# Performance work log

Measured on AMD Instinct MI355X. Metric: run time of the kernel, lower is better.

Reference implementation:

```python
import jax, jax.numpy as jnp
import numpy as np

N_NODES = 50000
N_EDGES = 800000
IN_CH, HID_CH, OUT_CH = 128, 128, 64


def _gcn_conv(x, W, b, src, dst, n):
    """PyG GCNConv: self-loops + symmetric norm + linear + scatter-add + bias."""
    loop = jnp.arange(n, dtype=src.dtype)
    src_sl = jnp.concatenate([src, loop])  # [E+N]
    dst_sl = jnp.concatenate([dst, loop])
    # degree computed on edges incl. self-loops (edge weight 1)
    deg = jax.ops.segment_sum(jnp.ones_like(dst_sl, dtype=x.dtype), dst_sl,
                              num_segments=n)
    dinv = jnp.where(deg > 0, jax.lax.rsqrt(deg), 0.0)
    norm = dinv[src_sl] * dinv[dst_sl]  # [E+N]
    xw = x @ W  # [N, F_out]
    msg = xw[src_sl] * norm[:, None]  # gather + scale, [E+N, F_out]
    out = jax.ops.segment_sum(msg, dst_sl, num_segments=n)
    return out + b


def setup_inputs() -> dict:
    key = jax.random.key(0)
    ks = jax.random.split(key, 5)
    x = jax.random.normal(ks[0], (N_NODES, IN_CH), dtype=jnp.float32)
    edge_index = jax.random.randint(ks[1], (2, N_EDGES), 0, N_NODES, dtype=jnp.int64)
    s1 = 1.0 / np.sqrt(IN_CH)
    s2 = 1.0 / np.sqrt(HID_CH)
    W1 = jax.random.normal(ks[2], (IN_CH, HID_CH), dtype=jnp.float32) * s1
    W2 = jax.random.normal(ks[3], (HID_CH, HID_CH), dtype=jnp.float32) * s2
    W3 = jax.random.normal(ks[4], (HID_CH, OUT_CH), dtype=jnp.float32) * s2
    return {
        "x": x, "edge_index": edge_index,
        "W1": W1, "b1": jnp.zeros((HID_CH,), jnp.float32),
        "W2": W2, "b2": jnp.zeros((HID_CH,), jnp.float32),
        "W3": W3, "b3": jnp.zeros((OUT_CH,), jnp.float32),
    }


def reference(x, edge_index, W1, b1, W2, b2, W3, b3):
    n = x.shape[0]
    src, dst = edge_index[0], edge_index[1]
    # dropout(p=0.6) is identity in eval mode
    h = jax.nn.relu(_gcn_conv(x, W1, b1, src, dst, n))
    h = jax.nn.relu(_gcn_conv(h, W2, b2, src, dst, n))
    out = _gcn_conv(h, W3, b3, src, dst, n)
    return out
```

## Files before the change

### kernel.cpp

```cpp
#include <hip/hip_runtime.h>
#include <cstdint>

#define CAP 32768
#define CHUNK 2048

typedef __attribute__((ext_vector_type(8))) short bf8_t;
typedef __attribute__((ext_vector_type(4))) float f4_t;

__device__ __forceinline__ uint32_t f_to_bf(float f) {
    union { float f; uint32_t u; } v; v.f = f;
    uint32_t u = v.u;
    return (u + 0x7fffu + ((u >> 16) & 1u)) >> 16;
}
__device__ __forceinline__ float bf_to_f(uint32_t h) {
    union { uint32_t u; float f; } v; v.u = h << 16; return v.f;
}
__device__ __forceinline__ float2 bf2_to_f2(uint32_t u) {
    union { uint32_t u; float f; } a, b;
    a.u = u << 16; b.u = u & 0xffff0000u;
    float2 r; r.x = a.f; r.y = b.f; return r;
}

__device__ __forceinline__ int detect64(const int* __restrict__ e32) {
    return (e32[1] | e32[3] | e32[5] | e32[7]) == 0;
}
__device__ __forceinline__ int edge_at(const void* edges, int is64, int idx) {
    if (is64) return (int)((const long long*)edges)[idx];
    return ((const int*)edges)[idx];
}

__global__ __launch_bounds__(256) void prep_kernel(
    const float* __restrict__ W1, const float* __restrict__ W2,
    const float* __restrict__ W3,
    uint16_t* w1h, uint16_t* w1l, uint16_t* w2h, uint16_t* w2l,
    uint16_t* w3h, uint16_t* w3l, int* __restrict__ bucket_cur) {
    if (blockIdx.x == 160) {
        if (threadIdx.x < 64) bucket_cur[threadIdx.x] = threadIdx.x * CAP;
        return;
    }
    int idx = blockIdx.x * 256 + threadIdx.x;
    const float* W; uint16_t* oh; uint16_t* ol; int FOUT; int e;
    if (idx < 16384)      { W = W1; oh = w1h; ol = w1l; FOUT = 128; e = idx; }
    else if (idx < 32768) { W = W2; oh = w2h; ol = w2l; FOUT = 128; e = idx - 16384; }
    else                  { W = W3; oh = w3h; ol = w3l; FOUT = 64;  e = idx - 32768; }
    int j = e & 7;
    int lane = (e >> 3) & 63;
    int rem = e >> 9;
    int NT = FOUT >> 4;
    int nt = rem % NT, kc = rem / NT;
    int k = kc * 32 + ((lane >> 4) << 3) + j;
    int c = nt * 16 + (lane & 15);
    float v = W[(size_t)k * FOUT + c];
    uint32_t h = f_to_bf(v);
    uint32_t l = f_to_bf(v - bf_to_f(h));
    oh[e] = (uint16_t)h;
    ol[e] = (uint16_t)l;
}

__device__ __forceinline__ void gemm1_body(
    const float* __restrict__ A, const uint16_t* __restrict__ Wfhi,
    const uint16_t* __restrict__ Wflo, uint16_t* __restrict__ Yout,
    int n, int cp, int tile0, int tstride, int lane) {
    constexpr int NT = 8, NTW = 2;
    int ntiles = (n + 15) >> 4;
    bf8_t wh[NTW][4], wl[NTW][4];
#pragma unroll
    for (int t = 0; t < NTW; t++) {
        int nt = cp * NTW + t;
#pragma unroll
        for (int kc = 0; kc < 4; kc++) {
            size_t b = ((size_t)(kc * NT + nt) * 64 + lane) * 8;
            wh[t][kc] = *(const bf8_t*)&Wfhi[b];
            wl[t][kc] = *(const bf8_t*)&Wflo[b];
        }
    }
    int row_in = lane & 15;
    int koff = (lane >> 4) << 3;
    int colb = lane & 15;
    int rq = (lane >> 4) << 2;
    for (int tile = tile0; tile < ntiles; tile += tstride) {
        int R = tile << 4;
        int arow = R + row_in; if (arow >= n) arow = n - 1;
        const float* ap = A + (size_t)arow * 128 + koff;
        bf8_t ah[4], al[4];
#pragma unroll
        for (int kc = 0; kc < 4; kc++) {
            float4 pv = *(const float4*)(ap + kc * 32);
            float4 qv = *(const float4*)(ap + kc * 32 + 4);
            float vv[8] = {pv.x, pv.y, pv.z, pv.w, qv.x, qv.y, qv.z, qv.w};
#pragma unroll
            for (int j = 0; j < 8; j++) {
                uint32_t h = f_to_bf(vv[j]);
                ah[kc][j] = (short)h;
                al[kc][j] = (short)f_to_bf(vv[j] - bf_to_f(h));
            }
        }
        f4_t acc[NTW];
#pragma unroll
        for (int t = 0; t < NTW; t++) acc[t] = (f4_t){0.f, 0.f, 0.f, 0.f};
#pragma unroll
        for (int kc = 0; kc < 4; kc++) {
#pragma unroll
            for (int t = 0; t < NTW; t++) {
                acc[t] = __builtin_amdgcn_mfma_f32_16x16x32_bf16(ah[kc], wh[t][kc], acc[t], 0, 0, 0);
                acc[t] = __builtin_amdgcn_mfma_f32_16x16x32_bf16(ah[kc], wl[t][kc], acc[t], 0, 0, 0);
                acc[t] = __builtin_amdgcn_mfma_f32_16x16x32_bf16(al[kc], wh[t][kc], acc[t], 0, 0, 0);
            }
        }
#pragma unroll
        for (int t = 0; t < NTW; t++) {
            int c = (cp * NTW + t) * 16 + colb;
#pragma unroll
            for (int r = 0; r < 4; r++) {
                int row = R + rq + r;
                if (row < n)
                    Yout[(size_t)row * 128 + c] = (uint16_t)f_to_bf(acc[t][r]);
            }
        }
    }
}

__global__ __launch_bounds__(256) void scatter_gemm1_kernel(
    const void* __restrict__ ei, int* __restrict__ bucket_cur,
    int2* __restrict__ buckets, int E, int sbcnt,
    const float* __restrict__ x, const uint16_t* __restrict__ w1h,
    const uint16_t* __restrict__ w1l, uint16_t* __restrict__ y1, int n) {
    int tid = threadIdx.x;
    if ((int)blockIdx.x < sbcnt) {
        __shared__ int cnt[64];
        int base = blockIdx.x * CHUNK;
        int is64 = detect64((const int*)ei);
        if (tid < 64) cnt[tid] = 0;
        __syncthreads();
        int dloc[8];
#pragma unroll
        for (int it = 0; it < 8; it++) {
            int i = base + it * 256 + tid;
            int d = (i < E) ? edge_at(ei, is64, E + i) : -1;
            dloc[it] = d;
            if (d >= 0) atomicAdd(&cnt[d >> 10], 1);
        }
        __syncthreads();
        if (tid < 64) {
            int v = cnt[tid];
            cnt[tid] = atomicAdd(&bucket_cur[tid], v);
        }
        __syncthreads();
#pragma unroll
        for (int it = 0; it < 8; it++) {
            int i = base + it * 256 + tid;
            if (dloc[it] >= 0) {
                int s = edge_at(ei, is64, i);
                int p = atomicAdd(&cnt[dloc[it] >> 10], 1);
                buckets[p] = make_int2(s, dloc[it]);
            }
        }
    } else {
        int lane = tid & 63, wid = tid >> 6;
        gemm1_body(x, w1h, w1l, y1, n, wid, blockIdx.x - sbcnt,
                   gridDim.x - sbcnt, lane);
    }
}

__global__ __launch_bounds__(512) void csr_local_kernel(
    const int2* __restrict__ buckets, const int* __restrict__ bucket_cur,
    int* __restrict__ row_ptr, int* __restrict__ bsum, float* __restrict__ dinv, int n) {
    __shared__ int cnt[1024];
    __shared__ int sb[1024];
    int b = blockIdx.x, tid = threadIdx.x;
    int base = b << 10;
    int lim = min(1024, n - base);
    if (lim <= 0) { if (tid == 0) bsum[b] = 0; return; }
    int ecnt = bucket_cur[b] - b * CAP;
    const int2* ebase = buckets + (size_t)b * CAP;
    for (int i = tid; i < 1024; i += 512) cnt[i] = 0;
    __syncthreads();
    for (int i = tid; i < ecnt; i += 512)
        atomicAdd(&cnt[ebase[i].y - base], 1);
    __syncthreads();
    for (int i = tid; i < lim; i += 512)
        dinv[base + i] = rsqrtf((float)(cnt[i] + 1));
    __syncthreads();
    int* a = cnt; int* s = sb;
    for (int st = 1; st < 1024; st <<= 1) {
        for (int i = tid; i < 1024; i += 512)
            s[i] = a[i] + ((i >= st) ? a[i - st] : 0);
        __syncthreads();
        int* t = a; a = s; s = t;
    }
    for (int i = tid; i < lim; i += 512)
        row_ptr[base + i] = (i > 0) ? a[i - 1] : 0;
    if (tid == 0) bsum[b] = a[1023];
}

__global__ void scan_totals_kernel(const int* __restrict__ bsum, int* __restrict__ boff,
                                   int* __restrict__ row_ptr, int nb, int n) {
    int lane = threadIdx.x;
    int v = (lane < nb) ? bsum[lane] : 0;
    int incl = v;
#pragma unroll
    for (int off = 1; off < 64; off <<= 1) {
        int t = __shfl_up(incl, off);
        if (lane >= off) incl += t;
    }
    if (lane < nb) boff[lane] = incl - v;
    if (lane == 63) row_ptr[n] = incl;
}

__global__ __launch_bounds__(512) void fill_bucket_kernel(
    const int2* __restrict__ buckets, const int* __restrict__ bucket_cur,
    int* __restrict__ row_ptr, const int* __restrict__ boff,
    int* __restrict__ col, int n) {
    __shared__ int cur[1024];
    int b = blockIdx.x, tid = threadIdx.x;
    int base = b << 10;
    int lim = min(1024, n - base);
    if (lim <= 0) return;
    int ecnt = bucket_cur[b] - b * CAP;
    const int2* ebase = buckets + (size_t)b * CAP;
    int bo = boff[b];
    for (int i = tid; i < lim; i += 512) {
        int v = row_ptr[base + i] + bo;
        row_ptr[base + i] = v;
        cur[i] = v;
    }
    __syncthreads();
    for (int i = tid; i < ecnt; i += 512) {
        int2 e = ebase[i];
        int p = atomicAdd(&cur[e.y - base], 1);
        col[p] = e.x;
    }
}

template <int FOUT, bool SRC_SCALE>
__global__ __launch_bounds__(256) void agg_gemm_kernel(
    const uint16_t* __restrict__ Yin, const int* __restrict__ row_ptr,
    const int* __restrict__ col, const float* __restrict__ dinv,
    const float* __restrict__ bias,
    const uint16_t* __restrict__ Wfhi, const uint16_t* __restrict__ Wflo,
    uint16_t* __restrict__ Yout, int n) {
    constexpr int LDW = 136;
    __shared__ uint16_t hs[16 * LDW];
    __shared__ uint16_t ls[16 * LDW];
    int tid = threadIdx.x, wid = tid >> 6, lane = tid & 63;
    int base = blockIdx.x * 16;

    auto lr = [&](int node) -> float2 {
        uint32_t u = ((const uint32_t*)Yin)[(size_t)node * 64 + lane];
        return bf2_to_f2(u);
    };

    for (int q = 0; q < 4; q++) {
        int r = wid * 4 + q, node = base + r;
        uint32_t ph = 0, pl = 0;
        if (node < n) {
            float di = dinv[node];
            float2 a0, a1, a2, a3;
            {
                float2 s = lr(node);
                float sc = SRC_SCALE ? di : 1.f;
                a0.x = s.x * sc; a0.y = s.y * sc;
            }
            a1 = (float2){0.f, 0.f}; a2 = (float2){0.f, 0.f}; a3 = (float2){0.f, 0.f};
            int start = row_ptr[node], end = row_ptr[node + 1];
            for (int b = start; b < end; b += 64) {
                int cnt = min(64, end - b);
                int sv = (b + lane < end) ? col[b + lane] : 0;
                int j = 0;
                for (; j + 4 <= cnt; j += 4) {
                    int s0 = __shfl(sv, j),     s1 = __shfl(sv, j + 1);
                    int s2 = __shfl(sv, j + 2), s3 = __shfl(sv, j + 3);
                    float d0 = 1.f, d1 = 1.f, d2 = 1.f, d3 = 1.f;
                    if (SRC_SCALE) { d0 = dinv[s0]; d1 = dinv[s1]; d2 = dinv[s2]; d3 = dinv[s3]; }
                    float2 v0 = lr(s0), v1 = lr(s1), v2 = lr(s2), v3 = lr(s3);
                    a0.x += v0.x * d0; a0.y += v0.y * d0;
                    a1.x += v1.x * d1; a1.y += v1.y * d1;
                    a2.x += v2.x * d2; a2.y += v2.y * d2;
                    a3.x += v3.x * d3; a3.y += v3.y * d3;
                }
                for (; j < cnt; j++) {
                    int s = __shfl(sv, j);
                    float d0 = SRC_SCALE ? dinv[s] : 1.f;
                    float2 v = lr(s);
                    a0.x += v.x * d0; a0.y += v.y * d0;
                }
            }
            float sx = (a0.x + a1.x) + (a2.x + a3.x);
            float sy = (a0.y + a1.y) + (a2.y + a3.y);
            float ox = fmaxf(sx * di + bias[2 * lane], 0.f);
            float oy = fmaxf(sy * di + bias[2 * lane + 1], 0.f);
            uint32_t h0 = f_to_bf(ox), h1 = f_to_bf(oy);
            uint32_t l0 = f_to_bf(ox - bf_to_f(h0)), l1 = f_to_bf(oy - bf_to_f(h1));
            ph = h0 | (h1 << 16); pl = l0 | (l1 << 16);
        }
        ((uint32_t*)(hs + r * LDW))[lane] = ph;
        ((uint32_t*)(ls + r * LDW))[lane] = pl;
    }
    __syncthreads();

    constexpr int NT = FOUT / 16;
    constexpr int NTW = NT / 4;
    int cp = wid;
    bf8_t wh[NTW][4], wl[NTW][4];
#pragma unroll
    for (int t = 0; t < NTW; t++) {
        int nt = cp * NTW + t;
#pragma unroll
        for (int kc = 0; kc < 4; kc++) {
            size_t b = ((size_t)(kc * NT + nt) * 64 + lane) * 8;
            wh[t][kc] = *(const bf8_t*)&Wfhi[b];
            wl[t][kc] = *(const bf8_t*)&Wflo[b];
        }
    }
    int koff = (lane >> 4) << 3;
    int colb = lane & 15;
    int rq = (lane >> 4) << 2;
    bf8_t ah[4], al[4];
#pragma unroll
    for (int kc = 0; kc < 4; kc++) {
        ah[kc] = *(const bf8_t*)(hs + (lane & 15) * LDW + koff + kc * 32);
        al[kc] = *(const bf8_t*)(ls + (lane & 15) * LDW + koff + kc * 32);
    }
    f4_t acc[NTW];
#pragma unroll
    for (int t = 0; t < NTW; t++) acc[t] = (f4_t){0.f, 0.f, 0.f, 0.f};
#pragma unroll
    for (int kc = 0; kc < 4; kc++) {
#pragma unroll
        for (int t = 0; t < NTW; t++) {
            acc[t] = __builtin_amdgcn_mfma_f32_16x16x32_bf16(ah[kc], wh[t][kc], acc[t], 0, 0, 0);
            acc[t] = __builtin_amdgcn_mfma_f32_16x16x32_bf16(ah[kc], wl[t][kc], acc[t], 0, 0, 0);
            acc[t] = __builtin_amdgcn_mfma_f32_16x16x32_bf16(al[kc], wh[t][kc], acc[t], 0, 0, 0);
        }
    }
#pragma unroll
    for (int t = 0; t < NTW; t++) {
        int c = (cp * NTW + t) * 16 + colb;
#pragma unroll
        for (int r = 0; r < 4; r++) {
            int row = base + rq + r;
            if (row < n) {
                float v = acc[t][r] * dinv[row];
                Yout[(size_t)row * FOUT + c] = (uint16_t)f_to_bf(v);
            }
        }
    }
}

__global__ __launch_bounds__(256) void agg_final_kernel(
    const uint16_t* __restrict__ Y, const int* __restrict__ row_ptr,
    const int* __restrict__ col, const float* __restrict__ dinv,
    const float* __restrict__ bias, float* __restrict__ out, int n) {
    int w = blockIdx.x * 4 + (threadIdx.x >> 6);
    int lane = threadIdx.x & 63;
    if (w >= n) return;
    auto lr = [&](int node) -> float {
        return bf_to_f(Y[(size_t)node * 64 + lane]);
    };
    float a0 = lr(w), a1 = 0.f, a2 = 0.f, a3 = 0.f;
    int start = row_ptr[w], end = row_ptr[w + 1];
    for (int b = start; b < end; b += 64) {
        int cnt = min(64, end - b);
        int sv = (b + lane < end) ? col[b + lane] : 0;
        int j = 0;
        for (; j + 4 <= cnt; j += 4) {
            int s0 = __shfl(sv, j),     s1 = __shfl(sv, j + 1);
            int s2 = __shfl(sv, j + 2), s3 = __shfl(sv, j + 3);
            a0 += lr(s0); a1 += lr(s1); a2 += lr(s2); a3 += lr(s3);
        }
        for (; j < cnt; j++) a0 += lr(__shfl(sv, j));
    }
    float ox = ((a0 + a1) + (a2 + a3)) * dinv[w] + bias[lane];
    out[(size_t)w * 64 + lane] = ox;
}

extern "C" void kernel_launch(void* const* d_in, const int* in_sizes, int n_in,
                              void* d_out, int out_size, void* d_ws, size_t ws_size,
                              hipStream_t stream) {
    const float* x  = (const float*)d_in[0];
    const void*  ei = d_in[1];
    const float* W1 = (const float*)d_in[2];
    const float* b1 = (const float*)d_in[3];
    const float* W2 = (const float*)d_in[4];
    const float* b2 = (const float*)d_in[5];
    const float* W3 = (const float*)d_in[6];
    const float* b3 = (const float*)d_in[7];
    int n = in_sizes[0] / 128;
    int E = in_sizes[1] / 2;
    int nbuck = (n + 1023) >> 10;

    char* p = (char*)d_ws;
    auto carve = [&](size_t bytes) {
        char* r = p;
        p += (bytes + 255) & ~(size_t)255;
        return r;
    };
    float*    dinv       = (float*)carve((size_t)n * 4);
    int*      row_ptr    = (int*)carve((size_t)(n + 1) * 4);
    int*      bsum       = (int*)carve(64 * 4);
    int*      boff       = (int*)carve(64 * 4);
    int*      bucket_cur = (int*)carve(64 * 4);
    int*      col        = (int*)carve((size_t)E * 4);
    int2*     buckets    = (int2*)carve((size_t)64 * CAP * 8);
    uint16_t* y1         = (uint16_t*)carve((size_t)n * 128 * 2);
    uint16_t* y2         = (uint16_t*)carve((size_t)n * 128 * 2);
    uint16_t* y3         = (uint16_t*)carve((size_t)n * 64 * 2);
    uint16_t* w1h        = (uint16_t*)carve(128 * 128 * 2);
    uint16_t* w1l        = (uint16_t*)carve(128 * 128 * 2);
    uint16_t* w2h        = (uint16_t*)carve(128 * 128 * 2);
    uint16_t* w2l        = (uint16_t*)carve(128 * 128 * 2);
    uint16_t* w3h        = (uint16_t*)carve(128 * 64 * 2);
    uint16_t* w3l        = (uint16_t*)carve(128 * 64 * 2);

    int sbcnt = (E + CHUNK - 1) / CHUNK;
    int fb = (n + 15) / 16;

    prep_kernel<<<161, 256, 0, stream>>>(W1, W2, W3, w1h, w1l, w2h, w2l,
                                         w3h, w3l, bucket_cur);
    scatter_gemm1_kernel<<<sbcnt + 782, 256, 0, stream>>>(
        ei, bucket_cur, buckets, E, sbcnt, x, w1h, w1l, y1, n);
    csr_local_kernel<<<nbuck, 512, 0, stream>>>(buckets, bucket_cur, row_ptr, bsum, dinv, n);
    scan_totals_kernel<<<1, 64, 0, stream>>>(bsum, boff, row_ptr, nbuck, n);
    fill_bucket_kernel<<<nbuck, 512, 0, stream>>>(buckets, bucket_cur, row_ptr, boff, col, n);
    agg_gemm_kernel<128, true><<<fb, 256, 0, stream>>>(
        y1, row_ptr, col, dinv, b1, w2h, w2l, y2, n);
    agg_gemm_kernel<64, false><<<fb, 256, 0, stream>>>(
        y2, row_ptr, col, dinv, b2, w3h, w3l, y3, n);
    agg_final_kernel<<<(n + 3) / 4, 256, 0, stream>>>(
        y3, row_ptr, col, dinv, b3, (float*)d_out, n);
}
```

Baseline: 248.4 us.

## Vectorize neighbor gathers with 16-byte loads and fold block scan into fill kernel

The aggregation kernels now have each lane load 8 bf16 features (uint4) per neighbor, with lane groups processing several neighbors at once and combining partial sums via cross-lane xor shuffles. This replaces narrow 4-byte (or 2-byte) per-lane gathers with wider transactions and more neighbors in flight per instruction. Separately, the tiny scan_totals launch is removed by having each fill_bucket block redo the 64-entry bucket prefix scan itself. The cost is extra shuffle reductions and masked lanes when neighbor counts are not multiples of the group size.

```diff
diff --git a/kernel.cpp b/kernel.cpp
--- a/kernel.cpp
+++ b/kernel.cpp
@@ -19,6 +19,14 @@
     union { uint32_t u; float f; } a, b;
     a.u = u << 16; b.u = u & 0xffff0000u;
     float2 r; r.x = a.f; r.y = b.f; return r;
+}
+__device__ __forceinline__ void fma8(float* acc, uint4 u, float d) {
+    float2 p0 = bf2_to_f2(u.x), p1 = bf2_to_f2(u.y);
+    float2 p2 = bf2_to_f2(u.z), p3 = bf2_to_f2(u.w);
+    acc[0] += p0.x * d; acc[1] += p0.y * d;
+    acc[2] += p1.x * d; acc[3] += p1.y * d;
+    acc[4] += p2.x * d; acc[5] += p2.y * d;
+    acc[6] += p3.x * d; acc[7] += p3.y * d;
 }
 
 __device__ __forceinline__ int detect64(const int* __restrict__ e32) {
@@ -193,32 +201,36 @@
     if (tid == 0) bsum[b] = a[1023];
 }
 
-__global__ void scan_totals_kernel(const int* __restrict__ bsum, int* __restrict__ boff,
-                                   int* __restrict__ row_ptr, int nb, int n) {
-    int lane = threadIdx.x;
-    int v = (lane < nb) ? bsum[lane] : 0;
-    int incl = v;
-#pragma unroll
-    for (int off = 1; off < 64; off <<= 1) {
-        int t = __shfl_up(incl, off);
-        if (lane >= off) incl += t;
-    }
-    if (lane < nb) boff[lane] = incl - v;
-    if (lane == 63) row_ptr[n] = incl;
-}
-
 __global__ __launch_bounds__(512) void fill_bucket_kernel(
     const int2* __restrict__ buckets, const int* __restrict__ bucket_cur,
-    int* __restrict__ row_ptr, const int* __restrict__ boff,
-    int* __restrict__ col, int n) {
+    int* __restrict__ row_ptr, const int* __restrict__ bsum,
+    int* __restrict__ col, int n, int nbuck) {
     __shared__ int cur[1024];
+    __shared__ int s_bo;
     int b = blockIdx.x, tid = threadIdx.x;
     int base = b << 10;
     int lim = min(1024, n - base);
     if (lim <= 0) return;
+    if (tid < 64) {
+        int lane = tid;
+        int v = (lane < nbuck) ? bsum[lane] : 0;
+        int incl = v;
+#pragma unroll
+        for (int off = 1; off < 64; off <<= 1) {
+            int t = __shfl_up(incl, off);
+            if (lane >= off) incl += t;
+        }
+        int tot = __shfl(incl, nbuck - 1);
+        int bo = (b > 0) ? __shfl(incl, b - 1) : 0;
+        if (lane == 0) {
+            s_bo = bo;
+            if (b == nbuck - 1) row_ptr[n] = tot;
+        }
+    }
+    __syncthreads();
     int ecnt = bucket_cur[b] - b * CAP;
     const int2* ebase = buckets + (size_t)b * CAP;
-    int bo = boff[b];
+    int bo = s_bo;
     for (int i = tid; i < lim; i += 512) {
         int v = row_ptr[base + i] + bo;
         row_ptr[base + i] = v;
@@ -239,67 +251,77 @@
     const float* __restrict__ bias,
     const uint16_t* __restrict__ Wfhi, const uint16_t* __restrict__ Wflo,
     uint16_t* __restrict__ Yout, int n) {
-    constexpr int LDW = 136;
-    __shared__ uint16_t hs[16 * LDW];
-    __shared__ uint16_t ls[16 * LDW];
+    __shared__ uint4 hs4[16 * 17];
+    __shared__ uint4 ls4[16 * 17];
     int tid = threadIdx.x, wid = tid >> 6, lane = tid & 63;
     int base = blockIdx.x * 16;
-
-    auto lr = [&](int node) -> float2 {
-        uint32_t u = ((const uint32_t*)Yin)[(size_t)node * 64 + lane];
-        return bf2_to_f2(u);
-    };
+    int g = lane & 15, j = lane >> 4;
+    const uint4* Y4 = (const uint4*)Yin;
+
+    float4 bb0 = *(const float4*)&bias[g * 8];
+    float4 bb1 = *(const float4*)&bias[g * 8 + 4];
+    float bb[8] = {bb0.x, bb0.y, bb0.z, bb0.w, bb1.x, bb1.y, bb1.z, bb1.w};
 
     for (int q = 0; q < 4; q++) {
         int r = wid * 4 + q, node = base + r;
-        uint32_t ph = 0, pl = 0;
+        uint4 ph = (uint4){0, 0, 0, 0}, pl = (uint4){0, 0, 0, 0};
         if (node < n) {
             float di = dinv[node];
-            float2 a0, a1, a2, a3;
+            float aA[8] = {}, aB[8] = {};
             {
-                float2 s = lr(node);
-                float sc = SRC_SCALE ? di : 1.f;
-                a0.x = s.x * sc; a0.y = s.y * sc;
-            }
-            a1 = (float2){0.f, 0.f}; a2 = (float2){0.f, 0.f}; a3 = (float2){0.f, 0.f};
+                float sd = (j == 0) ? (SRC_SCALE ? di : 1.f) : 0.f;
+                uint4 su = Y4[(size_t)node * 16 + g];
+                fma8(aA, su, sd);
+            }
             int start = row_ptr[node], end = row_ptr[node + 1];
             for (int b = start; b < end; b += 64) {
                 int cnt = min(64, end - b);
                 int sv = (b + lane < end) ? col[b + lane] : 0;
-                int j = 0;
-                for (; j + 4 <= cnt; j += 4) {
-                    int s0 = __shfl(sv, j),     s1 = __shfl(sv, j + 1);
-                    int s2 = __shfl(sv, j + 2), s3 = __shfl(sv, j + 3);
-                    float d0 = 1.f, d1 = 1.f, d2 = 1.f, d3 = 1.f;
-                    if (SRC_SCALE) { d0 = dinv[s0]; d1 = dinv[s1]; d2 = dinv[s2]; d3 = dinv[s3]; }
-                    float2 v0 = lr(s0), v1 = lr(s1), v2 = lr(s2), v3 = lr(s3);
-                    a0.x += v0.x * d0; a0.y += v0.y * d0;
-                    a1.x += v1.x * d1; a1.y += v1.y * d1;
-                    a2.x += v2.x * d2; a2.y += v2.y * d2;
-                    a3.x += v3.x * d3; a3.y += v3.y * d3;
+                for (int k = 0; k < cnt; k += 8) {
+                    int iA = k + j, iB = k + 4 + j;
+                    int sA = __shfl(sv, iA & 63);
+                    int sB = __shfl(sv, iB & 63);
+                    float dA = (iA < cnt) ? (SRC_SCALE ? dinv[sA] : 1.f) : 0.f;
+                    float dB = (iB < cnt) ? (SRC_SCALE ? dinv[sB] : 1.f) : 0.f;
+                    uint4 uA = Y4[(size_t)sA * 16 + g];
+                    uint4 uB = Y4[(size_t)sB * 16 + g];
+                    fma8(aA, uA, dA);
+                    fma8(aB, uB, dB);
                 }
-                for (; j < cnt; j++) {
-                    int s = __shfl(sv, j);
-                    float d0 = SRC_SCALE ? dinv[s] : 1.f;
-                    float2 v = lr(s);
-                    a0.x += v.x * d0; a0.y += v.y * d0;
-                }
-            }
-            float sx = (a0.x + a1.x) + (a2.x + a3.x);
-            float sy = (a0.y + a1.y) + (a2.y + a3.y);
-            float ox = fmaxf(sx * di + bias[2 * lane], 0.f);
-            float oy = fmaxf(sy * di + bias[2 * lane + 1], 0.f);
-            uint32_t h0 = f_to_bf(ox), h1 = f_to_bf(oy);
-            uint32_t l0 = f_to_bf(ox - bf_to_f(h0)), l1 = f_to_bf(oy - bf_to_f(h1));
-            ph = h0 | (h1 << 16); pl = l0 | (l1 << 16);
-        }
-        ((uint32_t*)(hs + r * LDW))[lane] = ph;
-        ((uint32_t*)(ls + r * LDW))[lane] = pl;
-    }
-    __syncthreads();
-
+            }
+            float o[8];
+#pragma unroll
+            for (int t = 0; t < 8; t++) o[t] = aA[t] + aB[t];
+#pragma unroll
+            for (int t = 0; t < 8; t++) o[t] += __shfl_xor(o[t], 16);
+#pragma unroll
+            for (int t = 0; t < 8; t++) o[t] += __shfl_xor(o[t], 32);
+            uint32_t hh[8];
+#pragma unroll
+            for (int t = 0; t < 8; t++) {
+                o[t] = fmaxf(o[t] * di + bb[t], 0.f);
+                hh[t] = f_to_bf(o[t]);
+            }
+            ph = (uint4){hh[0] | (hh[1] << 16), hh[2] | (hh[3] << 16),
+                         hh[4] | (hh[5] << 16), hh[6] | (hh[7] << 16)};
+            uint32_t ll[8];
+#pragma unroll
+            for (int t = 0; t < 8; t++) ll[t] = f_to_bf(o[t] - bf_to_f(hh[t]));
+            pl = (uint4){ll[0] | (ll[1] << 16), ll[2] | (ll[3] << 16),
+                         ll[4] | (ll[5] << 16), ll[6] | (ll[7] << 16)};
+        }
+        if (j == 0) {
+            hs4[r * 17 + g] = ph;
+            ls4[r * 17 + g] = pl;
+        }
+    }
+    __syncthreads();
+
+    const uint16_t* hs = (const uint16_t*)hs4;
+    const uint16_t* ls = (const uint16_t*)ls4;
     constexpr int NT = FOUT / 16;
     constexpr int NTW = NT / 4;
+    constexpr int LDW = 136;
     int cp = wid;
     bf8_t wh[NTW][4], wl[NTW][4];
 #pragma unroll
@@ -354,24 +376,51 @@
     int w = blockIdx.x * 4 + (threadIdx.x >> 6);
     int lane = threadIdx.x & 63;
     if (w >= n) return;
-    auto lr = [&](int node) -> float {
-        return bf_to_f(Y[(size_t)node * 64 + lane]);
-    };
-    float a0 = lr(w), a1 = 0.f, a2 = 0.f, a3 = 0.f;
+    int g = lane & 7, j = lane >> 3;
+    const uint4* Y4 = (const uint4*)Y;
+    float4 bb0 = *(const float4*)&bias[g * 8];
+    float4 bb1 = *(const float4*)&bias[g * 8 + 4];
+    float bb[8] = {bb0.x, bb0.y, bb0.z, bb0.w, bb1.x, bb1.y, bb1.z, bb1.w};
+
+    float aA[8] = {}, aB[8] = {};
+    {
+        uint4 su = Y4[(size_t)w * 8 + g];
+        fma8(aA, su, (j == 0) ? 1.f : 0.f);
+    }
     int start = row_ptr[w], end = row_ptr[w + 1];
     for (int b = start; b < end; b += 64) {
         int cnt = min(64, end - b);
         int sv = (b + lane < end) ? col[b + lane] : 0;
-        int j = 0;
-        for (; j + 4 <= cnt; j += 4) {
-            int s0 = __shfl(sv, j),     s1 = __shfl(sv, j + 1);
-            int s2 = __shfl(sv, j + 2), s3 = __shfl(sv, j + 3);
-            a0 += lr(s0); a1 += lr(s1); a2 += lr(s2); a3 += lr(s3);
-        }
-        for (; j < cnt; j++) a0 += lr(__shfl(sv, j));
-    }
-    float ox = ((a0 + a1) + (a2 + a3)) * dinv[w] + bias[lane];
-    out[(size_t)w * 64 + lane] = ox;
+        for (int k = 0; k < cnt; k += 16) {
+            int iA = k + j, iB = k + 8 + j;
+            int sA = __shfl(sv, iA & 63);
+            int sB = __shfl(sv, iB & 63);
+            float dA = (iA < cnt) ? 1.f : 0.f;
+            float dB = (iB < cnt) ? 1.f : 0.f;
+            uint4 uA = Y4[(size_t)sA * 8 + g];
+            uint4 uB = Y4[(size_t)sB * 8 + g];
+            fma8(aA, uA, dA);
+            fma8(aB, uB, dB);
+        }
+    }
+    float o[8];
+#pragma unroll
+    for (int t = 0; t < 8; t++) o[t] = aA[t] + aB[t];
+#pragma unroll
+    for (int t = 0; t < 8; t++) o[t] += __shfl_xor(o[t], 8);
+#pragma unroll
+    for (int t = 0; t < 8; t++) o[t] += __shfl_xor(o[t], 16);
+#pragma unroll
+    for (int t = 0; t < 8; t++) o[t] += __shfl_xor(o[t], 32);
+    float di = dinv[w];
+#pragma unroll
+    for (int t = 0; t < 8; t++) o[t] = o[t] * di + bb[t];
+    if (j == 0) {
+        float4 o0 = {o[0], o[1], o[2], o[3]};
+        float4 o1 = {o[4], o[5], o[6], o[7]};
+        *(float4*)&out[(size_t)w * 64 + g * 8] = o0;
+        *(float4*)&out[(size_t)w * 64 + g * 8 + 4] = o1;
+    }
 }
 
 extern "C" void kernel_launch(void* const* d_in, const int* in_sizes, int n_in,
@@ -398,7 +447,6 @@
     float*    dinv       = (float*)carve((size_t)n * 4);
     int*      row_ptr    = (int*)carve((size_t)(n + 1) * 4);
     int*      bsum       = (int*)carve(64 * 4);
-    int*      boff       = (int*)carve(64 * 4);
     int*      bucket_cur = (int*)carve(64 * 4);
     int*      col        = (int*)carve((size_t)E * 4);
     int2*     buckets    = (int2*)carve((size_t)64 * CAP * 8);
@@ -420,8 +468,8 @@
     scatter_gemm1_kernel<<<sbcnt + 782, 256, 0, stream>>>(
         ei, bucket_cur, buckets, E, sbcnt, x, w1h, w1l, y1, n);
     csr_local_kernel<<<nbuck, 512, 0, stream>>>(buckets, bucket_cur, row_ptr, bsum, dinv, n);
-    scan_totals_kernel<<<1, 64, 0, stream>>>(bsum, boff, row_ptr, nbuck, n);
-    fill_bucket_kernel<<<nbuck, 512, 0, stream>>>(buckets, bucket_cur, row_ptr, boff, col, n);
+    fill_bucket_kernel<<<nbuck, 512, 0, stream>>>(buckets, bucket_cur, row_ptr, bsum,
+                                                  col, n, nbuck);
     agg_gemm_kernel<128, true><<<fb, 256, 0, stream>>>(
         y1, row_ptr, col, dinv, b1, w2h, w2l, y2, n);
     agg_gemm_kernel<64, false><<<fb, 256, 0, stream>>>(
```

After: 243.6 us, median of 2. Within noise of the previous version (-1.9%).
